# Kernel optimization log

Measured on AMD Instinct MI355X. Metric: run time of the kernel, lower is better.

## Reference

```python
import jax, jax.numpy as jnp
import numpy as np

# Architecture constants (from init_kwargs)
IN_DIM, D_MODEL, HEADDIM, D_STATE, EXPAND, OUT_DIM = 57, 64, 32, 32, 2, 6
D_INNER = EXPAND * D_MODEL          # 128
NHEADS = D_INNER // HEADDIM         # 4
D_CONV = 4                          # causal depthwise conv width (mamba default)
D_XBC = D_INNER + 2 * D_STATE       # 192 (x, B, C share the conv)
D_IN_PROJ = 2 * D_INNER + 2 * D_STATE + NHEADS  # z, xBC, dt -> 324
BATCH, SEQ = 16, 2048


def setup_inputs() -> dict:
    key = jax.random.key(0)
    ks = jax.random.split(key, 12)
    s = 0.02
    return {
        "x": jax.random.normal(ks[0], (BATCH, SEQ, IN_DIM), jnp.float32),
        "W_lin": jax.random.normal(ks[1], (IN_DIM, D_MODEL), jnp.float32) * s,
        "b_lin": jnp.zeros((D_MODEL,), jnp.float32),
        "W_in": jax.random.normal(ks[2], (D_MODEL, D_IN_PROJ), jnp.float32) * s,
        "conv_w": jax.random.normal(ks[3], (D_XBC, 1, D_CONV), jnp.float32) * 0.5,
        "conv_b": jnp.zeros((D_XBC,), jnp.float32),
        "dt_bias": jnp.log(jax.random.uniform(ks[4], (NHEADS,), jnp.float32, 0.001, 0.1)),
        "A_log": jnp.log(jnp.arange(1, NHEADS + 1, dtype=jnp.float32)),
        "D": jnp.ones((NHEADS,), jnp.float32),
        "norm_w": jnp.ones((D_INNER,), jnp.float32),
        "W_out": jax.random.normal(ks[5], (D_INNER, D_MODEL), jnp.float32) * s,
        "W_cls": jax.random.normal(ks[6], (D_MODEL, OUT_DIM), jnp.float32) * s,
        "b_cls": jnp.zeros((OUT_DIM,), jnp.float32),
    }


def _mamba_block(h, W_in, conv_w, conv_b, dt_bias, A_log, D, norm_w, W_out):
    B, L, _ = h.shape
    zxbcdt = h @ W_in                                   # [B,L,324]
    z = zxbcdt[..., :D_INNER]                           # gate [B,L,128]
    xBC = zxbcdt[..., D_INNER:D_INNER + D_XBC]          # [B,L,192]
    dt = zxbcdt[..., D_INNER + D_XBC:]                  # [B,L,H]

    # causal depthwise conv over time + silu
    xBC = jax.lax.conv_general_dilated(
        xBC.transpose(0, 2, 1), conv_w, (1,), [(D_CONV - 1, 0)],
        dimension_numbers=("NCH", "OIH", "NCH"), feature_group_count=D_XBC)
    xBC = jax.nn.silu(xBC + conv_b[None, :, None]).transpose(0, 2, 1)

    xs = xBC[..., :D_INNER].reshape(B, L, NHEADS, HEADDIM)   # [B,L,H,P]
    Bm = xBC[..., D_INNER:D_INNER + D_STATE]                 # [B,L,N]
    Cm = xBC[..., D_INNER + D_STATE:]                        # [B,L,N]

    dt = jax.nn.softplus(dt + dt_bias)                       # [B,L,H]
    A = -jnp.exp(A_log)                                      # [H]

    def step(hstate, t):
        dtt, xt, bt, ct = t                                  # [B,H],[B,H,P],[B,N],[B,N]
        decay = jnp.exp(dtt * A)[:, :, None, None]           # [B,H,1,1]
        hstate = hstate * decay + (dtt[:, :, None] * xt)[..., None] * bt[:, None, None, :]
        y = jnp.einsum("bhpn,bn->bhp", hstate, ct)
        return hstate, y

    h0 = jnp.zeros((B, NHEADS, HEADDIM, D_STATE), h.dtype)
    _, ys = jax.lax.scan(step, h0, (dt.transpose(1, 0, 2), xs.transpose(1, 0, 2, 3),
                                    Bm.transpose(1, 0, 2), Cm.transpose(1, 0, 2)))
    y = ys.transpose(1, 0, 2, 3) + D[None, None, :, None] * xs   # [B,L,H,P]
    y = y.reshape(B, L, D_INNER)

    # gated RMSNorm + out proj
    y = y * jax.nn.silu(z)
    y = y * jax.lax.rsqrt(jnp.mean(y * y, axis=-1, keepdims=True) + 1e-5) * norm_w
    return y @ W_out                                        # [B,L,D_MODEL]


def reference(x, W_lin, b_lin, W_in, conv_w, conv_b, dt_bias, A_log, D, norm_w,
              W_out, W_cls, b_cls):
    h = x @ W_lin + b_lin                                   # linear_in
    h = _mamba_block(h, W_in, conv_w, conv_b, dt_bias, A_log, D, norm_w, W_out)
    pooled = h.mean(axis=1)                                 # AdaptiveAvgPool1d(1)
    return pooled @ W_cls + b_cls                           # classifier [B,6]
```

## Files before the change

kernel.cpp:

```cpp
#include <hip/hip_runtime.h>
#include <hip/hip_bf16.h>
#include <hip/hip_fp16.h>
#include <cmath>

#define BATCH   16
#define SEQ     2048
#define IN_DIM  57
#define D_MODEL 64
#define HEADDIM 32
#define D_STATE 32
#define OUT_DIM 6
#define D_INNER 128
#define NHEADS  4
#define D_CONV  4
#define D_XBC   192
#define D_XD    196
#define D_IN_PROJ 324
#define BL      (BATCH*SEQ)

#define NCHUNK  128
#define CLEN    (SEQ / NCHUNK)

#define RTILE   24
#define XPAD    60

#define OFF_WF   ((size_t)0)
#define OFF_BF   ((size_t)18496)
#define OFF_WOC  ((size_t)18848)
#define OFF_G    ((size_t)19744)
#define OFF_P    ((size_t)21792)
#define OFF_ZB   ((size_t)30016)
#define OFF_XD   (OFF_ZB + (size_t)BL*64)
#define OFF_SB   (OFF_XD + (size_t)BL*98)

__global__ void fuse_w_kernel(const float* __restrict__ W_lin,
                              const float* __restrict__ b_lin,
                              const float* __restrict__ W_in,
                              const float* __restrict__ W_out,
                              const float* __restrict__ W_cls,
                              float* __restrict__ Wf, float* __restrict__ bf,
                              float* __restrict__ Woc, float* __restrict__ G) {
    int idx = blockIdx.x * 256 + threadIdx.x;
    if (idx < BATCH * D_INNER) G[idx] = 0.f;
    if (idx < 58 * D_IN_PROJ) {
        int r = idx / D_IN_PROJ;
        int j = idx - r * D_IN_PROJ;
        const float* v = (r < IN_DIM) ? (W_lin + r * D_MODEL) : b_lin;
        float acc = 0.f;
#pragma unroll 8
        for (int m = 0; m < D_MODEL; ++m) acc += v[m] * W_in[m * D_IN_PROJ + j];
        if (r < IN_DIM) Wf[r * D_IN_PROJ + j] = acc;
        else            bf[j] = acc;
    } else if (idx < 58 * D_IN_PROJ + D_INNER * OUT_DIM) {
        int idx2 = idx - 58 * D_IN_PROJ;
        int i = idx2 / OUT_DIM;
        int o = idx2 - i * OUT_DIM;
        float acc = 0.f;
#pragma unroll 8
        for (int j = 0; j < D_MODEL; ++j)
            acc += W_out[i * D_MODEL + j] * W_cls[j * OUT_DIM + o];
        Woc[i * OUT_DIM + o] = acc;
    }
}

__global__ __launch_bounds__(256) void inproj_kernel(
        const float* __restrict__ x,
        const float* __restrict__ Wf,
        const float* __restrict__ bf,
        __half* __restrict__ zbh,
        __half* __restrict__ xdh) {
    __shared__ float xs[RTILE][XPAD];
    int r0 = blockIdx.x * RTILE;
    for (int i = threadIdx.x; i < RTILE * IN_DIM; i += 256) {
        size_t g = (size_t)r0 * IN_DIM + i;
        float v = (g < (size_t)BL * IN_DIM) ? x[g] : 0.f;
        xs[i / IN_DIM][i % IN_DIM] = v;
    }
    __syncthreads();
    if (threadIdx.x >= 243) return;
    int rset = threadIdx.x / 81;
    int cg   = threadIdx.x - rset * 81;
    int j0   = cg * 4;
    float4 bias = *(const float4*)(bf + j0);
    float4 acc[8];
#pragma unroll
    for (int r = 0; r < 8; ++r) acc[r] = bias;
    const float* w = Wf + j0;
    const float* xrow = &xs[rset * 8][0];
#pragma unroll 2
    for (int kc = 0; kc < 14; ++kc) {
        int k = kc * 4;
        float4 wv0 = *(const float4*)(w + (size_t)(k + 0) * D_IN_PROJ);
        float4 wv1 = *(const float4*)(w + (size_t)(k + 1) * D_IN_PROJ);
        float4 wv2 = *(const float4*)(w + (size_t)(k + 2) * D_IN_PROJ);
        float4 wv3 = *(const float4*)(w + (size_t)(k + 3) * D_IN_PROJ);
#pragma unroll
        for (int r = 0; r < 8; ++r) {
            float4 xv = *(const float4*)(xrow + r * XPAD + k);
            acc[r].x += xv.x * wv0.x + xv.y * wv1.x + xv.z * wv2.x + xv.w * wv3.x;
            acc[r].y += xv.x * wv0.y + xv.y * wv1.y + xv.z * wv2.y + xv.w * wv3.y;
            acc[r].z += xv.x * wv0.z + xv.y * wv1.z + xv.z * wv2.z + xv.w * wv3.z;
            acc[r].w += xv.x * wv0.w + xv.y * wv1.w + xv.z * wv2.w + xv.w * wv3.w;
        }
    }
    {
        float4 wv = *(const float4*)(w + (size_t)56 * D_IN_PROJ);
#pragma unroll
        for (int r = 0; r < 8; ++r) {
            float xv = xrow[r * XPAD + 56];
            acc[r].x += xv * wv.x; acc[r].y += xv * wv.y;
            acc[r].z += xv * wv.z; acc[r].w += xv * wv.w;
        }
    }
#pragma unroll
    for (int r = 0; r < 8; ++r) {
        int row = r0 + rset * 8 + r;
        if (row < BL) {
            __half2 h01 = __floats2half2_rn(acc[r].x, acc[r].y);
            __half2 h23 = __floats2half2_rn(acc[r].z, acc[r].w);
            uint2 u;
            u.x = *(unsigned*)&h01;
            u.y = *(unsigned*)&h23;
            if (j0 < D_INNER)
                *(uint2*)(zbh + (size_t)row * D_INNER + j0) = u;
            else
                *(uint2*)(xdh + (size_t)row * D_XD + (j0 - D_INNER)) = u;
        }
    }
}

__device__ __forceinline__ void conv_prologue(
        const __half* __restrict__ xdh,
        const float* __restrict__ conv_w, const float* __restrict__ conv_b,
        const float* __restrict__ dt_bias, const float* __restrict__ A_log,
        size_t rbase, int c, int tid,
        float (*xbt)[D_XBC], float (*ddl)[8]) {
    if (tid < D_XBC) {
        int ch = tid;
        float w0 = conv_w[ch*4+0], w1 = conv_w[ch*4+1];
        float w2 = conv_w[ch*4+2], w3 = conv_w[ch*4+3];
        float cb = conv_b[ch];
        const __half* src = xdh + rbase * D_XD + ch;
        float vm1 = 0.f, vm2 = 0.f, vm3 = 0.f;
        if (c > 0) {
            vm1 = __half2float(src[-(int)D_XD]);
            vm2 = __half2float(src[-2*(int)D_XD]);
            vm3 = __half2float(src[-3*(int)D_XD]);
        }
#pragma unroll
        for (int i = 0; i < CLEN; ++i) {
            float v0 = __half2float(src[(size_t)i * D_XD]);
            float a = cb + v0 * w3 + vm1 * w2 + vm2 * w1 + vm3 * w0;
            xbt[i][ch] = a / (1.f + expf(-a));
            vm3 = vm2; vm2 = vm1; vm1 = v0;
        }
    } else {
        int idx = tid - D_XBC;
        int h = idx >> 4, i = idx & 15;
        float v = __half2float(xdh[(rbase + i) * D_XD + 192 + h]) + dt_bias[h];
        float dtv = (v > 20.f) ? v : log1pf(expf(v));
        ddl[i][h * 2]     = dtv;
        ddl[i][h * 2 + 1] = expf(dtv * -expf(A_log[h]));
    }
}

__global__ __launch_bounds__(256) void scan_phase1_kernel(
        const __half* __restrict__ xdh,
        const float* __restrict__ conv_w, const float* __restrict__ conv_b,
        const float* __restrict__ dt_bias, const float* __restrict__ A_log,
        __half* __restrict__ sbuf, float* __restrict__ Pbuf) {
    int b = blockIdx.x >> 7;
    int c = blockIdx.x & 127;
    int tid = threadIdx.x;
    __shared__ float xbt[CLEN][D_XBC];
    __shared__ float ddl[CLEN][8];
    size_t rbase = (size_t)b * SEQ + (size_t)c * CLEN;
    conv_prologue(xdh, conv_w, conv_b, dt_bias, A_log, rbase, c, tid, xbt, ddl);
    __syncthreads();
    int h = tid >> 6, lane = tid & 63;
    int p = lane >> 1, n0 = (lane & 1) * 16;
    float4 s0 = make_float4(0.f,0.f,0.f,0.f), s1 = s0, s2 = s0, s3 = s0;
    float pacc = 1.f;
#pragma unroll 4
    for (int i = 0; i < CLEN; ++i) {
        float dtv = ddl[i][h * 2];
        float dec = ddl[i][h * 2 + 1];
        float xv = xbt[i][h * HEADDIM + p];
        const float* Bp = &xbt[i][D_INNER + n0];
        float4 B0 = *(const float4*)(Bp + 0);
        float4 B1 = *(const float4*)(Bp + 4);
        float4 B2 = *(const float4*)(Bp + 8);
        float4 B3 = *(const float4*)(Bp + 12);
        float coef = dtv * xv;
        s0.x = s0.x*dec + coef*B0.x; s0.y = s0.y*dec + coef*B0.y;
        s0.z = s0.z*dec + coef*B0.z; s0.w = s0.w*dec + coef*B0.w;
        s1.x = s1.x*dec + coef*B1.x; s1.y = s1.y*dec + coef*B1.y;
        s1.z = s1.z*dec + coef*B1.z; s1.w = s1.w*dec + coef*B1.w;
        s2.x = s2.x*dec + coef*B2.x; s2.y = s2.y*dec + coef*B2.y;
        s2.z = s2.z*dec + coef*B2.z; s2.w = s2.w*dec + coef*B2.w;
        s3.x = s3.x*dec + coef*B3.x; s3.y = s3.y*dec + coef*B3.y;
        s3.z = s3.z*dec + coef*B3.z; s3.w = s3.w*dec + coef*B3.w;
        pacc *= dec;
    }
    int bh = b * NHEADS + h;
    __half2 hs[8];
    hs[0] = __floats2half2_rn(s0.x, s0.y); hs[1] = __floats2half2_rn(s0.z, s0.w);
    hs[2] = __floats2half2_rn(s1.x, s1.y); hs[3] = __floats2half2_rn(s1.z, s1.w);
    hs[4] = __floats2half2_rn(s2.x, s2.y); hs[5] = __floats2half2_rn(s2.z, s2.w);
    hs[6] = __floats2half2_rn(s3.x, s3.y); hs[7] = __floats2half2_rn(s3.z, s3.w);
    uint4* sp = (uint4*)(sbuf + ((size_t)bh * NCHUNK + c) * 1024) + lane * 2;
    sp[0] = *(uint4*)&hs[0];
    sp[1] = *(uint4*)&hs[4];
    if (lane == 0) Pbuf[bh * NCHUNK + c] = pacc;
}

__global__ __launch_bounds__(256) void scan_phase2_kernel(
        __half* __restrict__ sbuf, const float* __restrict__ Pbuf) {
    int bh = blockIdx.x >> 1;
    int q  = blockIdx.x & 1;
    int idx = q * 256 + threadIdx.x;
    unsigned* s32 = (unsigned*)sbuf;
    float rx = 0.f, ry = 0.f;
#pragma unroll 8
    for (int c = 0; c < NCHUNK; ++c) {
        size_t a = ((size_t)bh * NCHUNK + c) * 512 + idx;
        unsigned v = s32[a];
        float Pv = Pbuf[bh * NCHUNK + c];
        __half2 hv = *(__half2*)&v;
        float2 t = __half22float2(hv);
        __half2 hr = __floats2half2_rn(rx, ry);
        s32[a] = *(unsigned*)&hr;
        rx = rx * Pv + t.x;
        ry = ry * Pv + t.y;
    }
}

__global__ __launch_bounds__(256) void scan_phase3_kernel(
        const __half* __restrict__ xdh,
        const float* __restrict__ conv_w, const float* __restrict__ conv_b,
        const float* __restrict__ dt_bias, const float* __restrict__ A_log,
        const __half* __restrict__ zbh, const float* __restrict__ Dp,
        const __half* __restrict__ sbuf, const float* __restrict__ norm_w,
        float* __restrict__ G) {
    int b = blockIdx.x >> 7;
    int c = blockIdx.x & 127;
    int tid = threadIdx.x;
    __shared__ float xbt[CLEN][D_XBC];
    __shared__ float ddl[CLEN][8];
    __shared__ float ylds[CLEN][D_INNER];
    __shared__ float red[4][D_INNER];
    size_t rbase = (size_t)b * SEQ + (size_t)c * CLEN;
    int h = tid >> 6, lane = tid & 63;
    int p = lane >> 1, n0 = (lane & 1) * 16;
    int bh = b * NHEADS + h;
    const uint4* sp = (const uint4*)(sbuf + ((size_t)bh * NCHUNK + c) * 1024) + lane * 2;
    uint4 u0 = sp[0], u1 = sp[1];
    float Dh = Dp[h];
    conv_prologue(xdh, conv_w, conv_b, dt_bias, A_log, rbase, c, tid, xbt, ddl);
    float4 s0, s1, s2, s3;
    {
        const __half2* hp0 = (const __half2*)&u0;
        const __half2* hp1 = (const __half2*)&u1;
        float2 f;
        f = __half22float2(hp0[0]); s0.x = f.x; s0.y = f.y;
        f = __half22float2(hp0[1]); s0.z = f.x; s0.w = f.y;
        f = __half22float2(hp0[2]); s1.x = f.x; s1.y = f.y;
        f = __half22float2(hp0[3]); s1.z = f.x; s1.w = f.y;
        f = __half22float2(hp1[0]); s2.x = f.x; s2.y = f.y;
        f = __half22float2(hp1[1]); s2.z = f.x; s2.w = f.y;
        f = __half22float2(hp1[2]); s3.x = f.x; s3.y = f.y;
        f = __half22float2(hp1[3]); s3.z = f.x; s3.w = f.y;
    }
    __syncthreads();
#pragma unroll 4
    for (int i = 0; i < CLEN; ++i) {
        float dtv = ddl[i][h * 2];
        float dec = ddl[i][h * 2 + 1];
        float xv = xbt[i][h * HEADDIM + p];
        const float* Bp = &xbt[i][D_INNER + n0];
        const float* Cp = &xbt[i][D_INNER + D_STATE + n0];
        float4 B0 = *(const float4*)(Bp + 0);
        float4 B1 = *(const float4*)(Bp + 4);
        float4 B2 = *(const float4*)(Bp + 8);
        float4 B3 = *(const float4*)(Bp + 12);
        float4 C0 = *(const float4*)(Cp + 0);
        float4 C1 = *(const float4*)(Cp + 4);
        float4 C2 = *(const float4*)(Cp + 8);
        float4 C3 = *(const float4*)(Cp + 12);
        float coef = dtv * xv;
        s0.x = s0.x*dec + coef*B0.x; s0.y = s0.y*dec + coef*B0.y;
        s0.z = s0.z*dec + coef*B0.z; s0.w = s0.w*dec + coef*B0.w;
        s1.x = s1.x*dec + coef*B1.x; s1.y = s1.y*dec + coef*B1.y;
        s1.z = s1.z*dec + coef*B1.z; s1.w = s1.w*dec + coef*B1.w;
        s2.x = s2.x*dec + coef*B2.x; s2.y = s2.y*dec + coef*B2.y;
        s2.z = s2.z*dec + coef*B2.z; s2.w = s2.w*dec + coef*B2.w;
        s3.x = s3.x*dec + coef*B3.x; s3.y = s3.y*dec + coef*B3.y;
        s3.z = s3.z*dec + coef*B3.z; s3.w = s3.w*dec + coef*B3.w;
        float part = s0.x*C0.x + s0.y*C0.y + s0.z*C0.z + s0.w*C0.w
                   + s1.x*C1.x + s1.y*C1.y + s1.z*C1.z + s1.w*C1.w
                   + s2.x*C2.x + s2.y*C2.y + s2.z*C2.z + s2.w*C2.w
                   + s3.x*C3.x + s3.y*C3.y + s3.z*C3.z + s3.w*C3.w;
        part += __shfl_xor(part, 1);
        if ((lane & 1) == 0)
            ylds[i][h * HEADDIM + p] = part + Dh * xv;
    }
    __syncthreads();
    float acc0 = 0.f, acc1 = 0.f;
    for (int r = h; r < CLEN; r += 4) {
        size_t bl = rbase + r;
        float2 yv = *(const float2*)(&ylds[r][lane * 2]);
        float2 zv = __half22float2(*((const __half2*)(zbh + bl * D_INNER) + lane));
        float g0 = yv.x * (zv.x / (1.f + expf(-zv.x)));
        float g1 = yv.y * (zv.y / (1.f + expf(-zv.y)));
        float sq = g0 * g0 + g1 * g1;
#pragma unroll
        for (int m = 1; m < 64; m <<= 1) sq += __shfl_xor(sq, m);
        float rms = 1.0f / sqrtf(sq * (1.f / 128.f) + 1e-5f);
        acc0 += g0 * rms;
        acc1 += g1 * rms;
    }
    red[h][lane * 2]     = acc0;
    red[h][lane * 2 + 1] = acc1;
    __syncthreads();
    if (tid < D_INNER) {
        float sg = red[0][tid] + red[1][tid] + red[2][tid] + red[3][tid];
        atomicAdd(&G[b * D_INNER + tid], sg * norm_w[tid]);
    }
}

__global__ void head_kernel(const float* __restrict__ G,
                            const float* __restrict__ Woc,
                            const float* __restrict__ b_cls,
                            float* __restrict__ out) {
    int tid = threadIdx.x;
    if (tid >= BATCH * OUT_DIM) return;
    int b = tid / OUT_DIM, o = tid - b * OUT_DIM;
    float acc = 0.f;
#pragma unroll 8
    for (int i = 0; i < D_INNER; ++i)
        acc += G[b * D_INNER + i] * Woc[i * OUT_DIM + o];
    out[b * OUT_DIM + o] = acc * (1.f / (float)SEQ) + b_cls[o];
}

extern "C" void kernel_launch(void* const* d_in, const int* in_sizes, int n_in,
                              void* d_out, int out_size, void* d_ws, size_t ws_size,
                              hipStream_t stream) {
    const float* x       = (const float*)d_in[0];
    const float* W_lin   = (const float*)d_in[1];
    const float* b_lin   = (const float*)d_in[2];
    const float* W_in    = (const float*)d_in[3];
    const float* conv_w  = (const float*)d_in[4];
    const float* conv_b  = (const float*)d_in[5];
    const float* dt_bias = (const float*)d_in[6];
    const float* A_log   = (const float*)d_in[7];
    const float* Dp      = (const float*)d_in[8];
    const float* norm_w  = (const float*)d_in[9];
    const float* W_out   = (const float*)d_in[10];
    const float* W_cls   = (const float*)d_in[11];
    const float* b_cls   = (const float*)d_in[12];
    float* out = (float*)d_out;

    float* ws = (float*)d_ws;
    float* Wf    = ws + OFF_WF;
    float* bf    = ws + OFF_BF;
    float* Woc   = ws + OFF_WOC;
    float* G     = ws + OFF_G;
    float* Pbuf  = ws + OFF_P;
    __half* zbh  = (__half*)(ws + OFF_ZB);
    __half* xdh  = (__half*)(ws + OFF_XD);
    __half* sbuf = (__half*)(ws + OFF_SB);

    fuse_w_kernel<<<(58 * D_IN_PROJ + D_INNER * OUT_DIM + 255) / 256, 256, 0, stream>>>(
        W_lin, b_lin, W_in, W_out, W_cls, Wf, bf, Woc, G);

    inproj_kernel<<<(BL + RTILE - 1) / RTILE, 256, 0, stream>>>(x, Wf, bf, zbh, xdh);

    scan_phase1_kernel<<<BATCH * NCHUNK, 256, 0, stream>>>(
        xdh, conv_w, conv_b, dt_bias, A_log, sbuf, Pbuf);
    scan_phase2_kernel<<<64 * 2, 256, 0, stream>>>(sbuf, Pbuf);
    scan_phase3_kernel<<<BATCH * NCHUNK, 256, 0, stream>>>(
        xdh, conv_w, conv_b, dt_bias, A_log, zbh, Dp, sbuf, norm_w, G);

    head_kernel<<<1, 128, 0, stream>>>(G, Woc, b_cls, out);
}
```

Baseline: 169.4 us.

## Compute intra-chunk outputs in phase 1 and add carried-state correction in phase 3

Phase 1 now runs the full local recurrence including the C readout, and stores the zero-initial-state outputs, C values and cumulative decays to global buffers in fp16/fp32. Phase 3 no longer redoes the conv and recurrence. It only adds the carried-in state's contribution, scaled by the cumulative decay, before gating and norm. The chunk count is halved, which lengthens each chunk and shrinks the sequential inter-chunk pass. The cost is extra global traffic for y, C and the decay buffers, fp16 rounding of y, and fewer blocks per scan kernel.

```diff
diff --git a/kernel.cpp b/kernel.cpp
--- a/kernel.cpp
+++ b/kernel.cpp
@@ -18,7 +18,7 @@
 #define D_IN_PROJ 324
 #define BL      (BATCH*SEQ)
 
-#define NCHUNK  128
+#define NCHUNK  64
 #define CLEN    (SEQ / NCHUNK)
 
 #define RTILE   24
@@ -29,9 +29,12 @@
 #define OFF_WOC  ((size_t)18848)
 #define OFF_G    ((size_t)19744)
 #define OFF_P    ((size_t)21792)
-#define OFF_ZB   ((size_t)30016)
+#define OFF_DC   ((size_t)25888)
+#define OFF_ZB   ((size_t)156960)
 #define OFF_XD   (OFF_ZB + (size_t)BL*64)
-#define OFF_SB   (OFF_XD + (size_t)BL*98)
+#define OFF_CB   (OFF_XD + (size_t)BL*98)
+#define OFF_YB   (OFF_CB + (size_t)BL*16)
+#define OFF_SB   (OFF_YB + (size_t)BL*64)
 
 __global__ void fuse_w_kernel(const float* __restrict__ W_lin,
                               const float* __restrict__ b_lin,
@@ -156,11 +159,17 @@
         }
     } else {
         int idx = tid - D_XBC;
-        int h = idx >> 4, i = idx & 15;
-        float v = __half2float(xdh[(rbase + i) * D_XD + 192 + h]) + dt_bias[h];
-        float dtv = (v > 20.f) ? v : log1pf(expf(v));
-        ddl[i][h * 2]     = dtv;
-        ddl[i][h * 2 + 1] = expf(dtv * -expf(A_log[h]));
+        int h = idx >> 4;
+        int i0 = idx & 15;
+        float db = dt_bias[h];
+        float nA = -expf(A_log[h]);
+#pragma unroll
+        for (int i = i0; i < CLEN; i += 16) {
+            float v = __half2float(xdh[(rbase + i) * D_XD + 192 + h]) + db;
+            float dtv = (v > 20.f) ? v : log1pf(expf(v));
+            ddl[i][h * 2]     = dtv;
+            ddl[i][h * 2 + 1] = expf(dtv * nA);
+        }
     }
 }
 
@@ -168,110 +177,25 @@
         const __half* __restrict__ xdh,
         const float* __restrict__ conv_w, const float* __restrict__ conv_b,
         const float* __restrict__ dt_bias, const float* __restrict__ A_log,
-        __half* __restrict__ sbuf, float* __restrict__ Pbuf) {
-    int b = blockIdx.x >> 7;
-    int c = blockIdx.x & 127;
+        const float* __restrict__ Dp,
+        __half* __restrict__ sbuf, float* __restrict__ Pbuf,
+        __half* __restrict__ ybuf, __half* __restrict__ Cbuf,
+        float* __restrict__ Dcum) {
+    int b = blockIdx.x >> 6;
+    int c = blockIdx.x & (NCHUNK - 1);
     int tid = threadIdx.x;
     __shared__ float xbt[CLEN][D_XBC];
     __shared__ float ddl[CLEN][8];
+    __shared__ __half yl[CLEN][D_INNER];
+    __shared__ float dcl[CLEN * 4];
     size_t rbase = (size_t)b * SEQ + (size_t)c * CLEN;
     conv_prologue(xdh, conv_w, conv_b, dt_bias, A_log, rbase, c, tid, xbt, ddl);
     __syncthreads();
     int h = tid >> 6, lane = tid & 63;
     int p = lane >> 1, n0 = (lane & 1) * 16;
+    float Dh = Dp[h];
     float4 s0 = make_float4(0.f,0.f,0.f,0.f), s1 = s0, s2 = s0, s3 = s0;
     float pacc = 1.f;
-#pragma unroll 4
-    for (int i = 0; i < CLEN; ++i) {
-        float dtv = ddl[i][h * 2];
-        float dec = ddl[i][h * 2 + 1];
-        float xv = xbt[i][h * HEADDIM + p];
-        const float* Bp = &xbt[i][D_INNER + n0];
-        float4 B0 = *(const float4*)(Bp + 0);
-        float4 B1 = *(const float4*)(Bp + 4);
-        float4 B2 = *(const float4*)(Bp + 8);
-        float4 B3 = *(const float4*)(Bp + 12);
-        float coef = dtv * xv;
-        s0.x = s0.x*dec + coef*B0.x; s0.y = s0.y*dec + coef*B0.y;
-        s0.z = s0.z*dec + coef*B0.z; s0.w = s0.w*dec + coef*B0.w;
-        s1.x = s1.x*dec + coef*B1.x; s1.y = s1.y*dec + coef*B1.y;
-        s1.z = s1.z*dec + coef*B1.z; s1.w = s1.w*dec + coef*B1.w;
-        s2.x = s2.x*dec + coef*B2.x; s2.y = s2.y*dec + coef*B2.y;
-        s2.z = s2.z*dec + coef*B2.z; s2.w = s2.w*dec + coef*B2.w;
-        s3.x = s3.x*dec + coef*B3.x; s3.y = s3.y*dec + coef*B3.y;
-        s3.z = s3.z*dec + coef*B3.z; s3.w = s3.w*dec + coef*B3.w;
-        pacc *= dec;
-    }
-    int bh = b * NHEADS + h;
-    __half2 hs[8];
-    hs[0] = __floats2half2_rn(s0.x, s0.y); hs[1] = __floats2half2_rn(s0.z, s0.w);
-    hs[2] = __floats2half2_rn(s1.x, s1.y); hs[3] = __floats2half2_rn(s1.z, s1.w);
-    hs[4] = __floats2half2_rn(s2.x, s2.y); hs[5] = __floats2half2_rn(s2.z, s2.w);
-    hs[6] = __floats2half2_rn(s3.x, s3.y); hs[7] = __floats2half2_rn(s3.z, s3.w);
-    uint4* sp = (uint4*)(sbuf + ((size_t)bh * NCHUNK + c) * 1024) + lane * 2;
-    sp[0] = *(uint4*)&hs[0];
-    sp[1] = *(uint4*)&hs[4];
-    if (lane == 0) Pbuf[bh * NCHUNK + c] = pacc;
-}
-
-__global__ __launch_bounds__(256) void scan_phase2_kernel(
-        __half* __restrict__ sbuf, const float* __restrict__ Pbuf) {
-    int bh = blockIdx.x >> 1;
-    int q  = blockIdx.x & 1;
-    int idx = q * 256 + threadIdx.x;
-    unsigned* s32 = (unsigned*)sbuf;
-    float rx = 0.f, ry = 0.f;
-#pragma unroll 8
-    for (int c = 0; c < NCHUNK; ++c) {
-        size_t a = ((size_t)bh * NCHUNK + c) * 512 + idx;
-        unsigned v = s32[a];
-        float Pv = Pbuf[bh * NCHUNK + c];
-        __half2 hv = *(__half2*)&v;
-        float2 t = __half22float2(hv);
-        __half2 hr = __floats2half2_rn(rx, ry);
-        s32[a] = *(unsigned*)&hr;
-        rx = rx * Pv + t.x;
-        ry = ry * Pv + t.y;
-    }
-}
-
-__global__ __launch_bounds__(256) void scan_phase3_kernel(
-        const __half* __restrict__ xdh,
-        const float* __restrict__ conv_w, const float* __restrict__ conv_b,
-        const float* __restrict__ dt_bias, const float* __restrict__ A_log,
-        const __half* __restrict__ zbh, const float* __restrict__ Dp,
-        const __half* __restrict__ sbuf, const float* __restrict__ norm_w,
-        float* __restrict__ G) {
-    int b = blockIdx.x >> 7;
-    int c = blockIdx.x & 127;
-    int tid = threadIdx.x;
-    __shared__ float xbt[CLEN][D_XBC];
-    __shared__ float ddl[CLEN][8];
-    __shared__ float ylds[CLEN][D_INNER];
-    __shared__ float red[4][D_INNER];
-    size_t rbase = (size_t)b * SEQ + (size_t)c * CLEN;
-    int h = tid >> 6, lane = tid & 63;
-    int p = lane >> 1, n0 = (lane & 1) * 16;
-    int bh = b * NHEADS + h;
-    const uint4* sp = (const uint4*)(sbuf + ((size_t)bh * NCHUNK + c) * 1024) + lane * 2;
-    uint4 u0 = sp[0], u1 = sp[1];
-    float Dh = Dp[h];
-    conv_prologue(xdh, conv_w, conv_b, dt_bias, A_log, rbase, c, tid, xbt, ddl);
-    float4 s0, s1, s2, s3;
-    {
-        const __half2* hp0 = (const __half2*)&u0;
-        const __half2* hp1 = (const __half2*)&u1;
-        float2 f;
-        f = __half22float2(hp0[0]); s0.x = f.x; s0.y = f.y;
-        f = __half22float2(hp0[1]); s0.z = f.x; s0.w = f.y;
-        f = __half22float2(hp0[2]); s1.x = f.x; s1.y = f.y;
-        f = __half22float2(hp0[3]); s1.z = f.x; s1.w = f.y;
-        f = __half22float2(hp1[0]); s2.x = f.x; s2.y = f.y;
-        f = __half22float2(hp1[1]); s2.z = f.x; s2.w = f.y;
-        f = __half22float2(hp1[2]); s3.x = f.x; s3.y = f.y;
-        f = __half22float2(hp1[3]); s3.z = f.x; s3.w = f.y;
-    }
-    __syncthreads();
 #pragma unroll 4
     for (int i = 0; i < CLEN; ++i) {
         float dtv = ddl[i][h * 2];
@@ -296,13 +220,128 @@
         s2.z = s2.z*dec + coef*B2.z; s2.w = s2.w*dec + coef*B2.w;
         s3.x = s3.x*dec + coef*B3.x; s3.y = s3.y*dec + coef*B3.y;
         s3.z = s3.z*dec + coef*B3.z; s3.w = s3.w*dec + coef*B3.w;
+        pacc *= dec;
         float part = s0.x*C0.x + s0.y*C0.y + s0.z*C0.z + s0.w*C0.w
                    + s1.x*C1.x + s1.y*C1.y + s1.z*C1.z + s1.w*C1.w
                    + s2.x*C2.x + s2.y*C2.y + s2.z*C2.z + s2.w*C2.w
                    + s3.x*C3.x + s3.y*C3.y + s3.z*C3.z + s3.w*C3.w;
         part += __shfl_xor(part, 1);
+        if (lane == 0) dcl[i * 4 + h] = pacc;
         if ((lane & 1) == 0)
-            ylds[i][h * HEADDIM + p] = part + Dh * xv;
+            yl[i][h * HEADDIM + p] = __float2half(part + Dh * xv);
+    }
+    int bh = b * NHEADS + h;
+    __half2 hs[8];
+    hs[0] = __floats2half2_rn(s0.x, s0.y); hs[1] = __floats2half2_rn(s0.z, s0.w);
+    hs[2] = __floats2half2_rn(s1.x, s1.y); hs[3] = __floats2half2_rn(s1.z, s1.w);
+    hs[4] = __floats2half2_rn(s2.x, s2.y); hs[5] = __floats2half2_rn(s2.z, s2.w);
+    hs[6] = __floats2half2_rn(s3.x, s3.y); hs[7] = __floats2half2_rn(s3.z, s3.w);
+    uint4* sp = (uint4*)(sbuf + ((size_t)bh * NCHUNK + c) * 1024) + lane * 2;
+    sp[0] = *(uint4*)&hs[0];
+    sp[1] = *(uint4*)&hs[4];
+    if (lane == 0) Pbuf[bh * NCHUNK + c] = pacc;
+    __syncthreads();
+    {
+        const uint4* ysrc = (const uint4*)&yl[0][0];
+        uint4* ydst = (uint4*)(ybuf + rbase * D_INNER);
+        ydst[tid]       = ysrc[tid];
+        ydst[tid + 256] = ysrc[tid + 256];
+    }
+    for (int idx = tid; idx < CLEN * 16; idx += 256) {
+        int r  = idx >> 4;
+        int n2 = (idx & 15) * 2;
+        __half2 hv = __floats2half2_rn(xbt[r][D_INNER + D_STATE + n2],
+                                       xbt[r][D_INNER + D_STATE + n2 + 1]);
+        *((__half2*)(Cbuf + (rbase + r) * D_STATE + n2)) = hv;
+    }
+    if (tid < CLEN * 4) Dcum[rbase * 4 + tid] = dcl[tid];
+}
+
+__global__ __launch_bounds__(256) void scan_phase2_kernel(
+        __half* __restrict__ sbuf, const float* __restrict__ Pbuf) {
+    int bh = blockIdx.x >> 1;
+    int q  = blockIdx.x & 1;
+    int idx = q * 256 + threadIdx.x;
+    unsigned* s32 = (unsigned*)sbuf;
+    float rx = 0.f, ry = 0.f;
+#pragma unroll 8
+    for (int c = 0; c < NCHUNK; ++c) {
+        size_t a = ((size_t)bh * NCHUNK + c) * 512 + idx;
+        unsigned v = s32[a];
+        float Pv = Pbuf[bh * NCHUNK + c];
+        __half2 hv = *(__half2*)&v;
+        float2 t = __half22float2(hv);
+        __half2 hr = __floats2half2_rn(rx, ry);
+        s32[a] = *(unsigned*)&hr;
+        rx = rx * Pv + t.x;
+        ry = ry * Pv + t.y;
+    }
+}
+
+__global__ __launch_bounds__(256) void scan_phase3_kernel(
+        const __half* __restrict__ ybuf, const __half* __restrict__ Cbuf,
+        const float* __restrict__ Dcum, const __half* __restrict__ zbh,
+        const __half* __restrict__ sbuf, const float* __restrict__ norm_w,
+        float* __restrict__ G) {
+    int b = blockIdx.x >> 6;
+    int c = blockIdx.x & (NCHUNK - 1);
+    int tid = threadIdx.x;
+    __shared__ float ylds[CLEN][D_INNER];
+    __shared__ float dcl[CLEN * 4];
+    __shared__ float red[4][D_INNER];
+    size_t rbase = (size_t)b * SEQ + (size_t)c * CLEN;
+    int h = tid >> 6, lane = tid & 63;
+    int p = lane >> 1, n0 = (lane & 1) * 16;
+    int bh = b * NHEADS + h;
+    const uint4* sp = (const uint4*)(sbuf + ((size_t)bh * NCHUNK + c) * 1024) + lane * 2;
+    uint4 u0 = sp[0], u1 = sp[1];
+    {
+        const __half2* ysrc = (const __half2*)(ybuf + rbase * D_INNER);
+        for (int idx = tid; idx < CLEN * D_INNER / 2; idx += 256) {
+            float2 f = __half22float2(ysrc[idx]);
+            int r  = idx >> 6;
+            int c2 = (idx & 63) * 2;
+            ylds[r][c2]     = f.x;
+            ylds[r][c2 + 1] = f.y;
+        }
+    }
+    if (tid < CLEN * 4) dcl[tid] = Dcum[rbase * 4 + tid];
+    float4 s0, s1, s2, s3;
+    {
+        const __half2* hp0 = (const __half2*)&u0;
+        const __half2* hp1 = (const __half2*)&u1;
+        float2 f;
+        f = __half22float2(hp0[0]); s0.x = f.x; s0.y = f.y;
+        f = __half22float2(hp0[1]); s0.z = f.x; s0.w = f.y;
+        f = __half22float2(hp0[2]); s1.x = f.x; s1.y = f.y;
+        f = __half22float2(hp0[3]); s1.z = f.x; s1.w = f.y;
+        f = __half22float2(hp1[0]); s2.x = f.x; s2.y = f.y;
+        f = __half22float2(hp1[1]); s2.z = f.x; s2.w = f.y;
+        f = __half22float2(hp1[2]); s3.x = f.x; s3.y = f.y;
+        f = __half22float2(hp1[3]); s3.z = f.x; s3.w = f.y;
+    }
+    __syncthreads();
+#pragma unroll 4
+    for (int i = 0; i < CLEN; ++i) {
+        const uint4* cp = (const uint4*)(Cbuf + (rbase + i) * D_STATE + n0);
+        uint4 ca = cp[0], cb = cp[1];
+        const __half2* cha = (const __half2*)&ca;
+        const __half2* chb = (const __half2*)&cb;
+        float2 f0 = __half22float2(cha[0]);
+        float2 f1 = __half22float2(cha[1]);
+        float2 f2 = __half22float2(cha[2]);
+        float2 f3 = __half22float2(cha[3]);
+        float2 f4 = __half22float2(chb[0]);
+        float2 f5 = __half22float2(chb[1]);
+        float2 f6 = __half22float2(chb[2]);
+        float2 f7 = __half22float2(chb[3]);
+        float part = s0.x*f0.x + s0.y*f0.y + s0.z*f1.x + s0.w*f1.y
+                   + s1.x*f2.x + s1.y*f2.y + s1.z*f3.x + s1.w*f3.y
+                   + s2.x*f4.x + s2.y*f4.y + s2.z*f5.x + s2.w*f5.y
+                   + s3.x*f6.x + s3.y*f6.y + s3.z*f7.x + s3.w*f7.y;
+        part += __shfl_xor(part, 1);
+        if ((lane & 1) == 0)
+            ylds[i][h * HEADDIM + p] += dcl[i * 4 + h] * part;
     }
     __syncthreads();
     float acc0 = 0.f, acc1 = 0.f;
@@ -366,8 +405,11 @@
     float* Woc   = ws + OFF_WOC;
     float* G     = ws + OFF_G;
     float* Pbuf  = ws + OFF_P;
+    float* Dcum  = ws + OFF_DC;
     __half* zbh  = (__half*)(ws + OFF_ZB);
     __half* xdh  = (__half*)(ws + OFF_XD);
+    __half* Cbh  = (__half*)(ws + OFF_CB);
+    __half* ybh  = (__half*)(ws + OFF_YB);
     __half* sbuf = (__half*)(ws + OFF_SB);
 
     fuse_w_kernel<<<(58 * D_IN_PROJ + D_INNER * OUT_DIM + 255) / 256, 256, 0, stream>>>(
@@ -376,10 +418,10 @@
     inproj_kernel<<<(BL + RTILE - 1) / RTILE, 256, 0, stream>>>(x, Wf, bf, zbh, xdh);
 
     scan_phase1_kernel<<<BATCH * NCHUNK, 256, 0, stream>>>(
-        xdh, conv_w, conv_b, dt_bias, A_log, sbuf, Pbuf);
+        xdh, conv_w, conv_b, dt_bias, A_log, Dp, sbuf, Pbuf, ybh, Cbh, Dcum);
     scan_phase2_kernel<<<64 * 2, 256, 0, stream>>>(sbuf, Pbuf);
     scan_phase3_kernel<<<BATCH * NCHUNK, 256, 0, stream>>>(
-        xdh, conv_w, conv_b, dt_bias, A_log, zbh, Dp, sbuf, norm_w, G);
+        ybh, Cbh, Dcum, zbh, sbuf, norm_w, G);
 
     head_kernel<<<1, 128, 0, stream>>>(G, Woc, b_cls, out);
 }
```

Result: no change. 168.4 us (-0.6%).
